# Kernel optimization log

Measured on AMD Instinct MI355X. Metric: run time of the kernel, lower is better.

## Reference

```python
import jax, jax.numpy as jnp
import numpy as np

B = 2
D = 256
NH = 8
DH = D // NH
LV = 4
NP_ = 4
NL = 6
DFF = 1024
SHAPES = [(112, 112), (56, 56), (28, 28), (14, 14)]
S = sum(h * w for h, w in SHAPES)


def setup_inputs() -> dict:
    key = jax.random.key(0)
    ks = iter(jax.random.split(key, 64))
    d = {}
    for i, (h, w) in enumerate(SHAPES):
        d[f"src{i}"] = jax.random.normal(next(ks), (B, D, h, w), jnp.float32)
        d[f"pos{i}"] = jax.random.normal(next(ks), (B, D, h, w), jnp.float32)

    def W(*shape, scale=0.02):
        return jax.random.normal(next(ks), shape, jnp.float32) * scale

    d["level_embed"] = W(LV, D, scale=1.0)
    d["off_w"] = W(NL, D, NH * LV * NP_ * 2)
    d["off_b"] = W(NL, NH * LV * NP_ * 2, scale=0.5)
    d["aw_w"] = W(NL, D, NH * LV * NP_)
    d["aw_b"] = jnp.zeros((NL, NH * LV * NP_), jnp.float32)
    d["val_w"] = W(NL, D, D)
    d["val_b"] = jnp.zeros((NL, D), jnp.float32)
    d["out_w"] = W(NL, D, D)
    d["out_b"] = jnp.zeros((NL, D), jnp.float32)
    d["ln1_s"] = jnp.ones((NL, D), jnp.float32)
    d["ln1_b"] = jnp.zeros((NL, D), jnp.float32)
    d["ff1_w"] = W(NL, D, DFF)
    d["ff1_b"] = jnp.zeros((NL, DFF), jnp.float32)
    d["ff2_w"] = W(NL, DFF, D)
    d["ff2_b"] = jnp.zeros((NL, D), jnp.float32)
    d["ln2_s"] = jnp.ones((NL, D), jnp.float32)
    d["ln2_b"] = jnp.zeros((NL, D), jnp.float32)
    return d


def _ln(x, s, b):
    m = jnp.mean(x, -1, keepdims=True)
    v = jnp.mean((x - m) ** 2, -1, keepdims=True)
    return (x - m) / jnp.sqrt(v + 1e-5) * s + b


def _bilinear(v, loc, Hl, Wl):
    # v: [N, DH, Hl, Wl]; loc: [N, Q, P, 2] in [0,1] (grid_sample align_corners=False, zero padding)
    N, Dh = v.shape[0], v.shape[1]
    Q, P = loc.shape[1], loc.shape[2]
    x = loc[..., 0] * Wl - 0.5
    y = loc[..., 1] * Hl - 0.5
    x0f = jnp.floor(x)
    y0f = jnp.floor(y)
    lx = x - x0f
    ly = y - y0f
    x0 = x0f.astype(jnp.int32)
    y0 = y0f.astype(jnp.int32)
    vf = v.reshape(N, Dh, Hl * Wl)

    def g(xi, yi):
        valid = (xi >= 0) & (xi < Wl) & (yi >= 0) & (yi < Hl)
        idx = (jnp.clip(yi, 0, Hl - 1) * Wl + jnp.clip(xi, 0, Wl - 1)).reshape(N, Q * P)
        out = jnp.take_along_axis(vf, idx[:, None, :], axis=2).reshape(N, Dh, Q, P)
        return out * valid[:, None].astype(v.dtype)

    w00 = ((1 - lx) * (1 - ly))[:, None]
    w10 = (lx * (1 - ly))[:, None]
    w01 = ((1 - lx) * ly)[:, None]
    w11 = (lx * ly)[:, None]
    return g(x0, y0) * w00 + g(x0 + 1, y0) * w10 + g(x0, y0 + 1) * w01 + g(x0 + 1, y0 + 1) * w11


def _ms_deform_attn(value, loc, attn):
    # value [B,S,NH,DH], loc [B,S,NH,LV,P,2], attn [B,S,NH,LV,P]
    out = jnp.zeros((B * NH, DH, S), value.dtype)
    s0 = 0
    for l, (Hl, Wl) in enumerate(SHAPES):
        vl = value[:, s0:s0 + Hl * Wl].reshape(B, Hl, Wl, NH, DH)
        vl = vl.transpose(0, 3, 4, 1, 2).reshape(B * NH, DH, Hl, Wl)
        ll = loc[:, :, :, l].transpose(0, 2, 1, 3, 4).reshape(B * NH, S, NP_, 2)
        al = attn[:, :, :, l].transpose(0, 2, 1, 3).reshape(B * NH, S, NP_)[:, None]
        out = out + (_bilinear(vl, ll, Hl, Wl) * al).sum(-1)
        s0 += Hl * Wl
    return out.reshape(B, NH * DH, S).transpose(0, 2, 1)


def _forward(srcs, poss, level_embed, off_w, off_b, aw_w, aw_b, val_w, val_b,
             out_w, out_b, ln1_s, ln1_b, ff1_w, ff1_b, ff2_w, ff2_b, ln2_s, ln2_b):
    src = jnp.concatenate([s.reshape(B, D, -1).transpose(0, 2, 1) for s in srcs], 1)
    pos = jnp.concatenate(
        [p.reshape(B, D, -1).transpose(0, 2, 1) + level_embed[i][None, None] for i, p in enumerate(poss)], 1)
    # reference points: padding masks are all-False => valid_ratios == 1
    refs = []
    for (Hl, Wl) in SHAPES:
        gy, gx = jnp.meshgrid((jnp.arange(Hl) + 0.5) / Hl, (jnp.arange(Wl) + 0.5) / Wl, indexing="ij")
        refs.append(jnp.stack([gx.ravel(), gy.ravel()], -1))
    ref = jnp.concatenate(refs, 0)  # [S, 2]
    normalizer = jnp.array([[w, h] for (h, w) in SHAPES], jnp.float32)  # [LV, 2] = (W, H)
    x = src
    for i in range(NL):
        q = x + pos
        off = (q @ off_w[i] + off_b[i]).reshape(B, S, NH, LV, NP_, 2)
        aw = jax.nn.softmax((q @ aw_w[i] + aw_b[i]).reshape(B, S, NH, LV * NP_), -1)
        aw = aw.reshape(B, S, NH, LV, NP_)
        val = (x @ val_w[i] + val_b[i]).reshape(B, S, NH, DH)
        loc = ref[None, :, None, None, None, :] + off / normalizer[None, None, None, :, None, :]
        attn_out = _ms_deform_attn(val, loc, aw) @ out_w[i] + out_b[i]
        x = _ln(x + attn_out, ln1_s[i], ln1_b[i])
        ff = jax.nn.relu(x @ ff1_w[i] + ff1_b[i]) @ ff2_w[i] + ff2_b[i]
        x = _ln(x + ff, ln2_s[i], ln2_b[i])
    return x


def reference(src0, src1, src2, src3, pos0, pos1, pos2, pos3, level_embed,
              off_w, off_b, aw_w, aw_b, val_w, val_b, out_w, out_b,
              ln1_s, ln1_b, ff1_w, ff1_b, ff2_w, ff2_b, ln2_s, ln2_b):
    memory = _forward([src0, src1, src2, src3], [pos0, pos1, pos2, pos3], level_embed,
                      off_w, off_b, aw_w, aw_b, val_w, val_b, out_w, out_b,
                      ln1_s, ln1_b, ff1_w, ff1_b, ff2_w, ff2_b, ln2_s, ln2_b)
    spatial_shapes = jnp.array(SHAPES, jnp.int32)
    level_start_index = jnp.concatenate(
        [jnp.zeros((1,), jnp.int32), jnp.cumsum(spatial_shapes.prod(1))[:-1].astype(jnp.int32)])
    return memory, spatial_shapes, level_start_index
```

## Files before the change

kernel.cpp:

```cpp
#include <hip/hip_runtime.h>


constexpr int kB  = 2;
constexpr int kD  = 256;
constexpr int kNH = 8;
constexpr int kLV = 4;
constexpr int kNP = 4;
constexpr int kNL = 6;
constexpr int kDFF = 1024;
constexpr int kS  = 16660;
constexpr int kM  = kB * kS;
constexpr int kMp = 33408;
constexpr int kMT64 = kMp / 64;

typedef short bf16x8 __attribute__((ext_vector_type(8)));
typedef float f32x4  __attribute__((ext_vector_type(4)));

__device__ __forceinline__ unsigned short f2bf(float x) {
  union { float f; unsigned int u; } v; v.f = x;
  unsigned int r = v.u + 0x7FFFu + ((v.u >> 16) & 1u);
  return (unsigned short)(r >> 16);
}
__device__ __forceinline__ float bf2f(unsigned short u) {
  union { unsigned int u; float f; } v; v.u = ((unsigned int)u) << 16;
  return v.f;
}
__device__ __forceinline__ float bflo(unsigned int u) {
  union { unsigned int u; float f; } v; v.u = u << 16;
  return v.f;
}
__device__ __forceinline__ float bfhi(unsigned int u) {
  union { unsigned int u; float f; } v; v.u = u & 0xFFFF0000u;
  return v.f;
}

#define GLOAD_LDS16(gp, lp)                                                    \
  __builtin_amdgcn_global_load_lds(                                            \
      (const __attribute__((address_space(1))) void*)(gp),                     \
      (__attribute__((address_space(3))) void*)(lp), 16, 0, 0)

#define SBARRIER() asm volatile("s_barrier" ::: "memory")

__global__ __launch_bounds__(256) void build_xpos_k(
    const float* __restrict__ src, const float* __restrict__ pos,
    const float* __restrict__ lemb, float* __restrict__ xout,
    unsigned short* __restrict__ posbf, unsigned short* __restrict__ xbf,
    unsigned short* __restrict__ qbf, int HW, int s0, int lvl)
{
  __shared__ float ts[32][33];
  __shared__ float tp[32][33];
  const int b  = blockIdx.z;
  const int p0 = blockIdx.x * 32, d0 = blockIdx.y * 32;
  const int tx = threadIdx.x, ty = threadIdx.y;
  for (int dd = ty; dd < 32; dd += 8) {
    int p = p0 + tx;
    if (p < HW) {
      size_t idx = ((size_t)b * kD + (d0 + dd)) * (size_t)HW + p;
      ts[dd][tx] = src[idx];
      tp[dd][tx] = pos[idx];
    }
  }
  __syncthreads();
  for (int pp = ty; pp < 32; pp += 8) {
    int p = p0 + pp, d = d0 + tx;
    if (p < HW) {
      size_t o = ((size_t)b * kS + (s0 + p)) * (size_t)kD + d;
      float x = ts[tx][pp];
      float pv = tp[tx][pp] + lemb[lvl * kD + d];
      xout[o] = x;
      posbf[o] = f2bf(pv);
      xbf[o] = f2bf(x);
      qbf[o] = f2bf(x + pv);
    }
  }
}

__global__ __launch_bounds__(256) void wconv_k(
    const float* __restrict__ W, unsigned short* __restrict__ Wt,
    int K, int N, int rowoff, int rowstotal)
{
  __shared__ float t[32][33];
  const int l = blockIdx.z;
  const int n0 = blockIdx.x * 32, k0 = blockIdx.y * 32;
  const int tx = threadIdx.x & 31, ty = threadIdx.x >> 5;
  const float* Wl = W + (size_t)l * K * N;
  unsigned short* Wtl = Wt + (size_t)l * rowstotal * K;
  for (int kk = ty; kk < 32; kk += 8)
    t[kk][tx] = Wl[(size_t)(k0 + kk) * N + n0 + tx];
  __syncthreads();
  for (int nn = ty; nn < 32; nn += 8)
    Wtl[(size_t)(rowoff + n0 + nn) * K + k0 + tx] = f2bf(t[tx][nn]);
}

__global__ __launch_bounds__(256) void biaspack_k(
    const float* __restrict__ ob, const float* __restrict__ ab,
    float* __restrict__ qb)
{
  int i = blockIdx.x * 256 + threadIdx.x;
  if (i >= kNL * 384) return;
  int l = i / 384, c = i - l * 384;
  qb[i] = (c < 256) ? ob[l * 256 + c] : ab[l * 128 + (c - 256)];
}

__global__ __launch_bounds__(256) void refxy_k(float* __restrict__ ref)
{
  int s = blockIdx.x * 256 + threadIdx.x;
  if (s >= kS) return;
  int ls, side;
  if (s < 12544)      { ls = s;         side = 112; }
  else if (s < 15680) { ls = s - 12544; side = 56;  }
  else if (s < 16464) { ls = s - 15680; side = 28;  }
  else                { ls = s - 16464; side = 14;  }
  const float inv = 1.0f / (float)side;
  ref[s * 2 + 0] = ((ls % side) + 0.5f) * inv;
  ref[s * 2 + 1] = ((ls / side) + 0.5f) * inv;
}

template<int RELU, int OUTBF>
__global__ __launch_bounds__(256) void hgemm64_k(
    const unsigned short* __restrict__ A, const unsigned short* __restrict__ Bt,
    const float* __restrict__ bias, void* __restrict__ Cout, int N, int K)
{
  __shared__ unsigned short As[2][64 * 32];
  __shared__ unsigned short Bs[2][128 * 32];
  const int tid = threadIdx.x;
  const int bm = blockIdx.y * 64;
  const int bn = blockIdx.x * 128;
  const int lane = tid & 63;
  const int wave = tid >> 6;
  const int wr = (wave >> 1) * 32, wc = (wave & 1) * 64;
  const int l15 = lane & 15, l4 = lane >> 4;

  f32x4 acc[2][4] = {};

  const unsigned short* A0 = A + (size_t)(bm + (tid >> 2)) * K + ((tid & 3) << 3);
  const int cb1 = 256 + tid;
  const unsigned short* B0 = Bt + (size_t)(bn + (tid >> 2)) * K + ((tid & 3) << 3);
  const unsigned short* B1 = Bt + (size_t)(bn + (cb1 >> 2)) * K + ((cb1 & 3) << 3);

#define STAGE64(buf, k0)                                                       \
  do {                                                                         \
    GLOAD_LDS16(A0 + (k0), (char*)As[buf] + tid * 16);                         \
    GLOAD_LDS16(B0 + (k0), (char*)Bs[buf] + tid * 16);                         \
    GLOAD_LDS16(B1 + (k0), (char*)Bs[buf] + cb1 * 16);                         \
  } while (0)

  const int nt = K >> 5;
  STAGE64(0, 0);
  STAGE64(1, 32);
  for (int k = 0; k < nt; ++k) {
    if (k + 1 < nt) asm volatile("s_waitcnt vmcnt(3)" ::: "memory");
    else            asm volatile("s_waitcnt vmcnt(0)" ::: "memory");
    SBARRIER();
    __builtin_amdgcn_sched_barrier(0);
    const int cur = k & 1;
    bf16x8 af[2], bfr[4];
#pragma unroll
    for (int m = 0; m < 2; ++m)
      af[m] = *(const bf16x8*)&As[cur][(wr + m * 16 + l15) * 32 + l4 * 8];
#pragma unroll
    for (int n = 0; n < 4; ++n)
      bfr[n] = *(const bf16x8*)&Bs[cur][(wc + n * 16 + l15) * 32 + l4 * 8];
#pragma unroll
    for (int m = 0; m < 2; ++m)
#pragma unroll
      for (int n = 0; n < 4; ++n)
        acc[m][n] = __builtin_amdgcn_mfma_f32_16x16x32_bf16(
            af[m], bfr[n], acc[m][n], 0, 0, 0);
    SBARRIER();
    if (k + 2 < nt) STAGE64(cur, (k + 2) * 32);
  }
#undef STAGE64

#pragma unroll
  for (int n = 0; n < 4; ++n) {
    const int col = bn + wc + n * 16 + l15;
    const float bv = bias[col];
#pragma unroll
    for (int m = 0; m < 2; ++m) {
#pragma unroll
      for (int j = 0; j < 4; ++j) {
        const int row = bm + wr + m * 16 + l4 * 4 + j;
        float v = acc[m][n][j] + bv;
        if (RELU) v = fmaxf(v, 0.f);
        if (OUTBF)
          ((unsigned short*)Cout)[(size_t)row * N + col] = f2bf(v);
        else
          ((float*)Cout)[(size_t)row * N + col] = v;
      }
    }
  }
}

__global__ __launch_bounds__(256) void qvgemm_k(
    const unsigned short* __restrict__ Aq, const unsigned short* __restrict__ Ax,
    const unsigned short* __restrict__ Bq, const unsigned short* __restrict__ Bv,
    const float* __restrict__ biasq, const float* __restrict__ biasv,
    _Float16* __restrict__ Cq, unsigned short* __restrict__ Cv)
{
  constexpr int K = 256;
  __shared__ unsigned short As[2][64 * 32];
  __shared__ unsigned short Bs[2][128 * 32];
  const int tid = threadIdx.x;
  const int bx = blockIdx.x;
  const bool isv = bx >= 3;
  const int bn = (isv ? bx - 3 : bx) * 128;
  const int bm = blockIdx.y * 64;
  const unsigned short* A  = isv ? Ax : Aq;
  const unsigned short* Bt = isv ? Bv : Bq;
  const float* bias = isv ? biasv : biasq;
  const int lane = tid & 63;
  const int wave = tid >> 6;
  const int wr = (wave >> 1) * 32, wc = (wave & 1) * 64;
  const int l15 = lane & 15, l4 = lane >> 4;

  f32x4 acc[2][4] = {};

  const unsigned short* A0 = A + (size_t)(bm + (tid >> 2)) * K + ((tid & 3) << 3);
  const int cb1 = 256 + tid;
  const unsigned short* B0 = Bt + (size_t)(bn + (tid >> 2)) * K + ((tid & 3) << 3);
  const unsigned short* B1 = Bt + (size_t)(bn + (cb1 >> 2)) * K + ((cb1 & 3) << 3);

#define STAGEQV(buf, k0)                                                       \
  do {                                                                         \
    GLOAD_LDS16(A0 + (k0), (char*)As[buf] + tid * 16);                         \
    GLOAD_LDS16(B0 + (k0), (char*)Bs[buf] + tid * 16);                         \
    GLOAD_LDS16(B1 + (k0), (char*)Bs[buf] + cb1 * 16);                         \
  } while (0)

  const int nt = K >> 5;
  STAGEQV(0, 0);
  STAGEQV(1, 32);
  for (int k = 0; k < nt; ++k) {
    if (k + 1 < nt) asm volatile("s_waitcnt vmcnt(3)" ::: "memory");
    else            asm volatile("s_waitcnt vmcnt(0)" ::: "memory");
    SBARRIER();
    __builtin_amdgcn_sched_barrier(0);
    const int cur = k & 1;
    bf16x8 af[2], bfr[4];
#pragma unroll
    for (int m = 0; m < 2; ++m)
      af[m] = *(const bf16x8*)&As[cur][(wr + m * 16 + l15) * 32 + l4 * 8];
#pragma unroll
    for (int n = 0; n < 4; ++n)
      bfr[n] = *(const bf16x8*)&Bs[cur][(wc + n * 16 + l15) * 32 + l4 * 8];
#pragma unroll
    for (int m = 0; m < 2; ++m)
#pragma unroll
      for (int n = 0; n < 4; ++n)
        acc[m][n] = __builtin_amdgcn_mfma_f32_16x16x32_bf16(
            af[m], bfr[n], acc[m][n], 0, 0, 0);
    SBARRIER();
    if (k + 2 < nt) STAGEQV(cur, (k + 2) * 32);
  }
#undef STAGEQV

#pragma unroll
  for (int n = 0; n < 4; ++n) {
    const int col = bn + wc + n * 16 + l15;
    const float bv = bias[col];
#pragma unroll
    for (int m = 0; m < 2; ++m) {
#pragma unroll
      for (int j = 0; j < 4; ++j) {
        const int row = bm + wr + m * 16 + l4 * 4 + j;
        float v = acc[m][n][j] + bv;
        if (isv)
          Cv[(size_t)row * 256 + col] = f2bf(v);
        else
          Cq[(size_t)row * 384 + col] = (_Float16)v;
      }
    }
  }
}

template<int WQ, int OUTDST>
__global__ __launch_bounds__(512) void hgemmln_k(
    const unsigned short* __restrict__ A, const unsigned short* __restrict__ Bt,
    const float* __restrict__ bias, const float* __restrict__ Rsd,
    const float* __restrict__ g, const float* __restrict__ beta,
    const unsigned short* __restrict__ posbf, float* __restrict__ yout,
    unsigned short* __restrict__ xbf, unsigned short* __restrict__ qbf, int K)
{
  __shared__ unsigned short As[2][64 * 32];
  __shared__ unsigned short Bs[2][256 * 32];
  float* ssum = (float*)&As[0][0];
  float* ssq  = ssum + 64 * 5;
  const int tid = threadIdx.x;
  const int bm = blockIdx.x * 64;
  const int lane = tid & 63;
  const int wave = tid >> 6;
  const int wm = wave >> 2;
  const int wn = wave & 3;
  const int wc = wn * 64;
  const int l15 = lane & 15, l4 = lane >> 4;

  f32x4 acc[2][4] = {};

  const unsigned short* Aq = A + (size_t)(bm + (tid >> 2)) * K + ((tid & 3) << 3);
  const unsigned short* Bq0 = Bt + (size_t)(tid >> 2) * K + ((tid & 3) << 3);
  const unsigned short* Bq1 = Bt + (size_t)(128 + (tid >> 2)) * K + ((tid & 3) << 3);

#define STAGE_LN(buf, k0)                                                      \
  do {                                                                         \
    if (tid < 256) GLOAD_LDS16(Aq + (k0), (char*)As[buf] + tid * 16);          \
    GLOAD_LDS16(Bq0 + (k0), (char*)Bs[buf] + tid * 16);                        \
    GLOAD_LDS16(Bq1 + (k0), (char*)Bs[buf] + (512 + tid) * 16);                \
  } while (0)

  const int nt = K >> 5;
  STAGE_LN(0, 0);
  STAGE_LN(1, 32);
  for (int k = 0; k < nt; ++k) {
    if (k + 1 < nt) {
      if (wave < 4) asm volatile("s_waitcnt vmcnt(3)" ::: "memory");
      else          asm volatile("s_waitcnt vmcnt(2)" ::: "memory");
    } else {
      asm volatile("s_waitcnt vmcnt(0)" ::: "memory");
    }
    SBARRIER();
    __builtin_amdgcn_sched_barrier(0);
    const int cur = k & 1;
    bf16x8 af[2], bfr[4];
#pragma unroll
    for (int m = 0; m < 2; ++m)
      af[m] = *(const bf16x8*)&As[cur][(wm * 32 + m * 16 + l15) * 32 + l4 * 8];
#pragma unroll
    for (int n = 0; n < 4; ++n)
      bfr[n] = *(const bf16x8*)&Bs[cur][(wc + n * 16 + l15) * 32 + l4 * 8];
#pragma unroll
    for (int m = 0; m < 2; ++m)
#pragma unroll
      for (int n = 0; n < 4; ++n)
        acc[m][n] = __builtin_amdgcn_mfma_f32_16x16x32_bf16(
            af[m], bfr[n], acc[m][n], 0, 0, 0);
    SBARRIER();
    if (k + 2 < nt) STAGE_LN(cur, (k + 2) * 32);
  }
#undef STAGE_LN

  float bv[4], gv[4], btv[4];
#pragma unroll
  for (int n = 0; n < 4; ++n) {
    const int col = wc + n * 16 + l15;
    bv[n] = bias[col];
    gv[n] = g[col];
    btv[n] = beta[col];
  }
#pragma unroll
  for (int m = 0; m < 2; ++m) {
#pragma unroll
    for (int j = 0; j < 4; ++j) {
      const int row = bm + wm * 32 + m * 16 + l4 * 4 + j;
#pragma unroll
      for (int n = 0; n < 4; ++n)
        acc[m][n][j] += bv[n] + Rsd[(size_t)row * kD + wc + n * 16 + l15];
    }
  }
#pragma unroll
  for (int m = 0; m < 2; ++m) {
#pragma unroll
    for (int j = 0; j < 4; ++j) {
      float s = acc[m][0][j] + acc[m][1][j] + acc[m][2][j] + acc[m][3][j];
      float q = acc[m][0][j] * acc[m][0][j] + acc[m][1][j] * acc[m][1][j] +
                acc[m][2][j] * acc[m][2][j] + acc[m][3][j] * acc[m][3][j];
#pragma unroll
      for (int d2 = 1; d2 < 16; d2 <<= 1) {
        s += __shfl_xor(s, d2, 64);
        q += __shfl_xor(q, d2, 64);
      }
      if (l15 == 0) {
        const int r = wm * 32 + m * 16 + l4 * 4 + j;
        ssum[r * 5 + wn] = s;
        ssq[r * 5 + wn] = q;
      }
    }
  }
  __syncthreads();
#pragma unroll
  for (int m = 0; m < 2; ++m) {
#pragma unroll
    for (int j = 0; j < 4; ++j) {
      const int r = wm * 32 + m * 16 + l4 * 4 + j;
      const int row = bm + r;
      const float mean = (ssum[r * 5 + 0] + ssum[r * 5 + 1] + ssum[r * 5 + 2] +
                          ssum[r * 5 + 3]) * (1.0f / kD);
      const float var = (ssq[r * 5 + 0] + ssq[r * 5 + 1] + ssq[r * 5 + 2] +
                         ssq[r * 5 + 3]) * (1.0f / kD) - mean * mean;
      const float rstd = rsqrtf(var + 1e-5f);
      if (row < kM) {
#pragma unroll
        for (int n = 0; n < 4; ++n) {
          const int col = wc + n * 16 + l15;
          const float y = (acc[m][n][j] - mean) * rstd * gv[n] + btv[n];
          const size_t o = (size_t)row * kD + col;
          if (OUTDST) {
            yout[o] = y;
          } else {
            yout[o] = y;
            xbf[o] = f2bf(y);
            if (WQ) qbf[o] = f2bf(y + bf2f(posbf[o]));
          }
        }
      }
    }
  }
}

__global__ __launch_bounds__(256) void msdeform_k(
    const unsigned short* __restrict__ val, const _Float16* __restrict__ qout,
    const float* __restrict__ ref, unsigned short* __restrict__ outbf)
{
  __shared__ int   sIdx[4][8][128];
  __shared__ float sW[4][8][128];
  const int bid = blockIdx.x;
  const int xcd = bid & 7;
  const int jj  = bid >> 3;
  const int wg  = (xcd < 5 ? xcd * 521 : 5 * 521 + (xcd - 5) * 520) + jj;
  const int bs0 = wg * 8;
  const int tid = threadIdx.x;

#pragma unroll
  for (int it = 0; it < 4; ++it) {
    const int item = tid + it * 256;
    const int q = item >> 7;
    const int t = item & 127;
    const int bs = bs0 + q;
    const int b = bs / kS, s = bs - b * kS;
    const int l = (t & 15) >> 2;

    const float logit = (float)qout[(size_t)bs * 384 + 256 + t];
    float mx = logit;
#pragma unroll
    for (int d2 = 1; d2 < 16; d2 <<= 1) mx = fmaxf(mx, __shfl_xor(mx, d2, 64));
    float e = __expf(logit - mx);
    float sm = e;
#pragma unroll
    for (int d2 = 1; d2 < 16; d2 <<= 1) sm += __shfl_xor(sm, d2, 64);
    const float a = e / sm;

    const float rfx = ref[s * 2 + 0];
    const float rfy = ref[s * 2 + 1];
    const int side  = 112 >> l;
    const int start = (l >= 1 ? 12544 : 0) + (l >= 2 ? 3136 : 0) + (l >= 3 ? 784 : 0);
    const float ox = (float)qout[(size_t)bs * 384 + t * 2 + 0];
    const float oy = (float)qout[(size_t)bs * 384 + t * 2 + 1];
    const float xx = fmaf(rfx, (float)side, ox) - 0.5f;
    const float yy = fmaf(rfy, (float)side, oy) - 0.5f;
    const float xf = floorf(xx), yf = floorf(yy);
    const float lx = xx - xf, ly = yy - yf;
    const int x0 = (int)xf, y0 = (int)yf;
    const float w00 = (1.f - lx) * (1.f - ly) * a, w10 = lx * (1.f - ly) * a;
    const float w01 = (1.f - lx) * ly * a,         w11 = lx * ly * a;
    const bool xv0 = (unsigned)x0 < (unsigned)side, xv1 = (unsigned)(x0 + 1) < (unsigned)side;
    const bool yv0 = (unsigned)y0 < (unsigned)side, yv1 = (unsigned)(y0 + 1) < (unsigned)side;
    const int cx0 = min(max(x0, 0), side - 1), cx1 = min(max(x0 + 1, 0), side - 1);
    const int cy0 = min(max(y0, 0), side - 1), cy1 = min(max(y0 + 1, 0), side - 1);
    const int rowbase = b * kS + start;
    const int t2 = (t & 15) * 8 + (t >> 4);
    sIdx[0][q][t2] = (rowbase + cy0 * side + cx0) << 9;
    sIdx[1][q][t2] = (rowbase + cy0 * side + cx1) << 9;
    sIdx[2][q][t2] = (rowbase + cy1 * side + cx0) << 9;
    sIdx[3][q][t2] = (rowbase + cy1 * side + cx1) << 9;
    sW[0][q][t2] = (xv0 && yv0) ? w00 : 0.f;
    sW[1][q][t2] = (xv1 && yv0) ? w10 : 0.f;
    sW[2][q][t2] = (xv0 && yv1) ? w01 : 0.f;
    sW[3][q][t2] = (xv1 && yv1) ? w11 : 0.f;
  }
  __syncthreads();

  const int q  = tid >> 5;
  const int h  = (tid >> 2) & 7;
  const int l4 = tid & 3;
  const char* vbase = (const char*)val + h * 64 + l4 * 16;

  float a0 = 0.f, a1 = 0.f, a2 = 0.f, a3 = 0.f;
  float a4 = 0.f, a5 = 0.f, a6 = 0.f, a7 = 0.f;
#pragma unroll
  for (int sp = 0; sp < 16; ++sp) {
    const int t2 = sp * 8 + h;
#pragma unroll
    for (int c = 0; c < 4; ++c) {
      const int off = sIdx[c][q][t2];
      const float w = sW[c][q][t2];
      const uint4 v = *(const uint4*)(vbase + off);
      a0 = fmaf(w, bflo(v.x), a0); a1 = fmaf(w, bfhi(v.x), a1);
      a2 = fmaf(w, bflo(v.y), a2); a3 = fmaf(w, bfhi(v.y), a3);
      a4 = fmaf(w, bflo(v.z), a4); a5 = fmaf(w, bfhi(v.z), a5);
      a6 = fmaf(w, bflo(v.w), a6); a7 = fmaf(w, bfhi(v.w), a7);
    }
  }
  bf16x8 o;
  o[0] = (short)f2bf(a0); o[1] = (short)f2bf(a1);
  o[2] = (short)f2bf(a2); o[3] = (short)f2bf(a3);
  o[4] = (short)f2bf(a4); o[5] = (short)f2bf(a5);
  o[6] = (short)f2bf(a6); o[7] = (short)f2bf(a7);
  *(bf16x8*)(outbf + (size_t)(bs0 + q) * 256 + h * 32 + l4 * 8) = o;
}

__global__ void tail_k(float* __restrict__ out)
{
  if (threadIdx.x == 0) {
    const size_t n = (size_t)kM * kD;
    out[n + 0] = 112.f; out[n + 1] = 112.f;
    out[n + 2] = 56.f;  out[n + 3] = 56.f;
    out[n + 4] = 28.f;  out[n + 5] = 28.f;
    out[n + 6] = 14.f;  out[n + 7] = 14.f;
    out[n + 8] = 0.f;   out[n + 9] = 12544.f;
    out[n + 10] = 15680.f; out[n + 11] = 16464.f;
  }
}

extern "C" void kernel_launch(void* const* d_in, const int* in_sizes, int n_in,
                              void* d_out, int out_size, void* d_ws, size_t ws_size,
                              hipStream_t stream)
{
  const float* src[4] = {(const float*)d_in[0], (const float*)d_in[2],
                         (const float*)d_in[4], (const float*)d_in[6]};
  const float* pos[4] = {(const float*)d_in[1], (const float*)d_in[3],
                         (const float*)d_in[5], (const float*)d_in[7]};
  const float* lemb  = (const float*)d_in[8];
  const float* off_w = (const float*)d_in[9];
  const float* off_b = (const float*)d_in[10];
  const float* aw_w  = (const float*)d_in[11];
  const float* aw_b  = (const float*)d_in[12];
  const float* val_w = (const float*)d_in[13];
  const float* val_b = (const float*)d_in[14];
  const float* out_w = (const float*)d_in[15];
  const float* out_b = (const float*)d_in[16];
  const float* ln1_s = (const float*)d_in[17];
  const float* ln1_b = (const float*)d_in[18];
  const float* ff1_w = (const float*)d_in[19];
  const float* ff1_b = (const float*)d_in[20];
  const float* ff2_w = (const float*)d_in[21];
  const float* ff2_b = (const float*)d_in[22];
  const float* ln2_s = (const float*)d_in[23];
  const float* ln2_b = (const float*)d_in[24];

  const size_t SZ = (size_t)kMp * kD;
  float* ws   = (float*)d_ws;
  float* xb   = ws;
  _Float16* qoutH = (_Float16*)(ws + SZ);
  unsigned short* valbf = (unsigned short*)(ws + SZ + (3 * SZ) / 4);
  unsigned short* attbf = valbf + SZ;
  unsigned short* ffbf  = (unsigned short*)(ws + SZ);
  unsigned short* posbf = (unsigned short*)(ws + 3 * SZ);
  unsigned short* qbf   = posbf + SZ;
  unsigned short* xbf   = qbf + SZ;
  unsigned short* wts   = (unsigned short*)(ws + 4 * SZ + SZ / 2);
  unsigned short* qwT  = wts;
  unsigned short* valT = qwT + kNL * 384 * 256;
  unsigned short* outT = valT + kNL * 256 * 256;
  unsigned short* ff1T = outT + kNL * 256 * 256;
  unsigned short* ff2T = ff1T + kNL * 1024 * 256;
  float* qbias = (float*)(ff2T + kNL * 256 * 1024);
  float* reftab = qbias + kNL * 384;

  wconv_k<<<dim3(256 / 32, 256 / 32, kNL), 256, 0, stream>>>(off_w, qwT, 256, 256, 0, 384);
  wconv_k<<<dim3(128 / 32, 256 / 32, kNL), 256, 0, stream>>>(aw_w,  qwT, 256, 128, 256, 384);
  wconv_k<<<dim3(256 / 32, 256 / 32, kNL), 256, 0, stream>>>(val_w, valT, 256, 256, 0, 256);
  wconv_k<<<dim3(256 / 32, 256 / 32, kNL), 256, 0, stream>>>(out_w, outT, 256, 256, 0, 256);
  wconv_k<<<dim3(1024 / 32, 256 / 32, kNL), 256, 0, stream>>>(ff1_w, ff1T, 256, 1024, 0, 1024);
  wconv_k<<<dim3(256 / 32, 1024 / 32, kNL), 256, 0, stream>>>(ff2_w, ff2T, 1024, 256, 0, 256);
  biaspack_k<<<(kNL * 384 + 255) / 256, 256, 0, stream>>>(off_b, aw_b, qbias);
  refxy_k<<<(kS + 255) / 256, 256, 0, stream>>>(reftab);

  const int sides[4]  = {112, 56, 28, 14};
  const int starts[4] = {0, 12544, 15680, 16464};
  for (int l = 0; l < 4; ++l) {
    int HW = sides[l] * sides[l];
    dim3 g((HW + 31) / 32, kD / 32, kB);
    build_xpos_k<<<g, dim3(32, 8), 0, stream>>>(src[l], pos[l], lemb, xb, posbf,
                                                xbf, qbf, HW, starts[l], l);
  }

  const dim3 blk(256);
  for (int i = 0; i < kNL; ++i) {
    qvgemm_k<<<dim3(5, kMT64), blk, 0, stream>>>(
        qbf, xbf, qwT + (size_t)i * 384 * 256, valT + (size_t)i * 256 * 256,
        qbias + i * 384, val_b + i * 256, qoutH, valbf);
    msdeform_k<<<kM / 8, blk, 0, stream>>>(valbf, qoutH, reftab, attbf);
    hgemmln_k<0, 0><<<kMT64, 512, 0, stream>>>(
        attbf, outT + (size_t)i * 256 * 256, out_b + i * 256, xb,
        ln1_s + i * kD, ln1_b + i * kD, nullptr, xb, xbf, nullptr, 256);
    hgemm64_k<1, 1><<<dim3(8, kMT64), blk, 0, stream>>>(
        xbf, ff1T + (size_t)i * 1024 * 256, ff1_b + i * 1024, ffbf, 1024, 256);
    if (i < kNL - 1) {
      hgemmln_k<1, 0><<<kMT64, 512, 0, stream>>>(
          ffbf, ff2T + (size_t)i * 256 * 1024, ff2_b + i * 256, xb,
          ln2_s + i * kD, ln2_b + i * kD, posbf, xb, xbf, qbf, 1024);
    } else {
      hgemmln_k<0, 1><<<kMT64, 512, 0, stream>>>(
          ffbf, ff2T + (size_t)i * 256 * 1024, ff2_b + i * 256, xb,
          ln2_s + i * kD, ln2_b + i * kD, nullptr, (float*)d_out, nullptr,
          nullptr, 1024);
    }
  }

  tail_k<<<1, 64, 0, stream>>>((float*)d_out);
}
```

Baseline: 1.357 ms.

## Deepen hgemmln K-loop pipeline to four LDS stages with split MFMA phases

The GEMM+LayerNorm kernel moves from a double-buffered to a four-stage LDS ring, issuing global-to-LDS loads up to three k-steps ahead with computed vmcnt waits. Each k-step is split into two MFMA phases separated by barriers, with explicit lgkmcnt waits and setprio raised around the MFMA bursts so waves interleave memory and compute. This aims to hide global load latency better. In exchange it doubles the shared memory footprint, which may lower occupancy, and adds more barriers per iteration.

Measured after the change: 1.410 ms. 3.9% more time.

```diff
diff --git a/kernel.cpp b/kernel.cpp
--- a/kernel.cpp
+++ b/kernel.cpp
@@ -40,6 +40,22 @@
       (__attribute__((address_space(3))) void*)(lp), 16, 0, 0)
 
 #define SBARRIER() asm volatile("s_barrier" ::: "memory")
+#define LGKM0()                                                                \
+  do {                                                                         \
+    asm volatile("s_waitcnt lgkmcnt(0)" ::: "memory");                         \
+    __builtin_amdgcn_sched_barrier(0);                                         \
+  } while (0)
+
+__device__ __forceinline__ void vmwait(int n) {
+  switch (n) {
+    case 0: asm volatile("s_waitcnt vmcnt(0)" ::: "memory"); break;
+    case 2: asm volatile("s_waitcnt vmcnt(2)" ::: "memory"); break;
+    case 3: asm volatile("s_waitcnt vmcnt(3)" ::: "memory"); break;
+    case 4: asm volatile("s_waitcnt vmcnt(4)" ::: "memory"); break;
+    case 6: asm volatile("s_waitcnt vmcnt(6)" ::: "memory"); break;
+    default: asm volatile("s_waitcnt vmcnt(9)" ::: "memory"); break;
+  }
+}
 
 __global__ __launch_bounds__(256) void build_xpos_k(
     const float* __restrict__ src, const float* __restrict__ pos,
@@ -282,8 +298,8 @@
     const unsigned short* __restrict__ posbf, float* __restrict__ yout,
     unsigned short* __restrict__ xbf, unsigned short* __restrict__ qbf, int K)
 {
-  __shared__ unsigned short As[2][64 * 32];
-  __shared__ unsigned short Bs[2][256 * 32];
+  __shared__ unsigned short As[4][64 * 32];
+  __shared__ unsigned short Bs[4][256 * 32];
   float* ssum = (float*)&As[0][0];
   float* ssq  = ssum + 64 * 5;
   const int tid = threadIdx.x;
@@ -301,43 +317,87 @@
   const unsigned short* Bq0 = Bt + (size_t)(tid >> 2) * K + ((tid & 3) << 3);
   const unsigned short* Bq1 = Bt + (size_t)(128 + (tid >> 2)) * K + ((tid & 3) << 3);
 
-#define STAGE_LN(buf, k0)                                                      \
+#define ISSUE(h)                                                               \
   do {                                                                         \
-    if (tid < 256) GLOAD_LDS16(Aq + (k0), (char*)As[buf] + tid * 16);          \
-    GLOAD_LDS16(Bq0 + (k0), (char*)Bs[buf] + tid * 16);                        \
-    GLOAD_LDS16(Bq1 + (k0), (char*)Bs[buf] + (512 + tid) * 16);                \
+    const int _s = (h) & 3;                                                    \
+    const int _k = (h) * 32;                                                   \
+    GLOAD_LDS16(Bq0 + _k, (char*)Bs[_s] + tid * 16);                           \
+    GLOAD_LDS16(Bq1 + _k, (char*)Bs[_s] + (512 + tid) * 16);                   \
+    if (tid < 256) GLOAD_LDS16(Aq + _k, (char*)As[_s] + tid * 16);             \
   } while (0)
 
-  const int nt = K >> 5;
-  STAGE_LN(0, 0);
-  STAGE_LN(1, 32);
-  for (int k = 0; k < nt; ++k) {
-    if (k + 1 < nt) {
-      if (wave < 4) asm volatile("s_waitcnt vmcnt(3)" ::: "memory");
-      else          asm volatile("s_waitcnt vmcnt(2)" ::: "memory");
-    } else {
-      asm volatile("s_waitcnt vmcnt(0)" ::: "memory");
-    }
-    SBARRIER();
+  const int NT = K >> 6;
+  const int HL = 2 * NT - 1;
+  const int Lw = (wave < 4) ? 3 : 2;
+
+  ISSUE(0);
+  ISSUE(1);
+  ISSUE(2);
+
+  for (int T = 0; T < NT; ++T) {
+    const int h0 = 2 * T, h1 = 2 * T + 1;
+    const int s0 = h0 & 3, s1 = h1 & 3;
+    bf16x8 af0, af1, b0, b1, b2, b3;
+
+    if (h0 + 3 <= HL) ISSUE(h0 + 3);
+    vmwait(((h0 + 3 <= HL ? h0 + 3 : HL) - h0) * Lw);
+    SBARRIER();
+    af0 = *(const bf16x8*)&As[s0][(wm * 32 + 0 * 16 + l15) * 32 + l4 * 8];
+    af1 = *(const bf16x8*)&As[s0][(wm * 32 + 1 * 16 + l15) * 32 + l4 * 8];
+    b0  = *(const bf16x8*)&Bs[s0][(wc + 0 * 16 + l15) * 32 + l4 * 8];
+    b1  = *(const bf16x8*)&Bs[s0][(wc + 1 * 16 + l15) * 32 + l4 * 8];
+    LGKM0();
+    __builtin_amdgcn_s_setprio(1);
+    acc[0][0] = __builtin_amdgcn_mfma_f32_16x16x32_bf16(af0, b0, acc[0][0], 0, 0, 0);
+    acc[1][0] = __builtin_amdgcn_mfma_f32_16x16x32_bf16(af1, b0, acc[1][0], 0, 0, 0);
+    acc[0][1] = __builtin_amdgcn_mfma_f32_16x16x32_bf16(af0, b1, acc[0][1], 0, 0, 0);
+    acc[1][1] = __builtin_amdgcn_mfma_f32_16x16x32_bf16(af1, b1, acc[1][1], 0, 0, 0);
+    __builtin_amdgcn_s_setprio(0);
     __builtin_amdgcn_sched_barrier(0);
-    const int cur = k & 1;
-    bf16x8 af[2], bfr[4];
-#pragma unroll
-    for (int m = 0; m < 2; ++m)
-      af[m] = *(const bf16x8*)&As[cur][(wm * 32 + m * 16 + l15) * 32 + l4 * 8];
-#pragma unroll
-    for (int n = 0; n < 4; ++n)
-      bfr[n] = *(const bf16x8*)&Bs[cur][(wc + n * 16 + l15) * 32 + l4 * 8];
-#pragma unroll
-    for (int m = 0; m < 2; ++m)
-#pragma unroll
-      for (int n = 0; n < 4; ++n)
-        acc[m][n] = __builtin_amdgcn_mfma_f32_16x16x32_bf16(
-            af[m], bfr[n], acc[m][n], 0, 0, 0);
-    SBARRIER();
-    if (k + 2 < nt) STAGE_LN(cur, (k + 2) * 32);
-  }
-#undef STAGE_LN
+    SBARRIER();
+
+    b2 = *(const bf16x8*)&Bs[s0][(wc + 2 * 16 + l15) * 32 + l4 * 8];
+    b3 = *(const bf16x8*)&Bs[s0][(wc + 3 * 16 + l15) * 32 + l4 * 8];
+    LGKM0();
+    __builtin_amdgcn_s_setprio(1);
+    acc[0][2] = __builtin_amdgcn_mfma_f32_16x16x32_bf16(af0, b2, acc[0][2], 0, 0, 0);
+    acc[1][2] = __builtin_amdgcn_mfma_f32_16x16x32_bf16(af1, b2, acc[1][2], 0, 0, 0);
+    acc[0][3] = __builtin_amdgcn_mfma_f32_16x16x32_bf16(af0, b3, acc[0][3], 0, 0, 0);
+    acc[1][3] = __builtin_amdgcn_mfma_f32_16x16x32_bf16(af1, b3, acc[1][3], 0, 0, 0);
+    __builtin_amdgcn_s_setprio(0);
+    __builtin_amdgcn_sched_barrier(0);
+    SBARRIER();
+
+    if (h0 + 4 <= HL) ISSUE(h0 + 4);
+    vmwait(((h0 + 4 <= HL ? h0 + 4 : HL) - h1) * Lw);
+    SBARRIER();
+    af0 = *(const bf16x8*)&As[s1][(wm * 32 + 0 * 16 + l15) * 32 + l4 * 8];
+    af1 = *(const bf16x8*)&As[s1][(wm * 32 + 1 * 16 + l15) * 32 + l4 * 8];
+    b0  = *(const bf16x8*)&Bs[s1][(wc + 0 * 16 + l15) * 32 + l4 * 8];
+    b1  = *(const bf16x8*)&Bs[s1][(wc + 1 * 16 + l15) * 32 + l4 * 8];
+    LGKM0();
+    __builtin_amdgcn_s_setprio(1);
+    acc[0][0] = __builtin_amdgcn_mfma_f32_16x16x32_bf16(af0, b0, acc[0][0], 0, 0, 0);
+    acc[1][0] = __builtin_amdgcn_mfma_f32_16x16x32_bf16(af1, b0, acc[1][0], 0, 0, 0);
+    acc[0][1] = __builtin_amdgcn_mfma_f32_16x16x32_bf16(af0, b1, acc[0][1], 0, 0, 0);
+    acc[1][1] = __builtin_amdgcn_mfma_f32_16x16x32_bf16(af1, b1, acc[1][1], 0, 0, 0);
+    __builtin_amdgcn_s_setprio(0);
+    __builtin_amdgcn_sched_barrier(0);
+    SBARRIER();
+
+    b2 = *(const bf16x8*)&Bs[s1][(wc + 2 * 16 + l15) * 32 + l4 * 8];
+    b3 = *(const bf16x8*)&Bs[s1][(wc + 3 * 16 + l15) * 32 + l4 * 8];
+    LGKM0();
+    __builtin_amdgcn_s_setprio(1);
+    acc[0][2] = __builtin_amdgcn_mfma_f32_16x16x32_bf16(af0, b2, acc[0][2], 0, 0, 0);
+    acc[1][2] = __builtin_amdgcn_mfma_f32_16x16x32_bf16(af1, b2, acc[1][2], 0, 0, 0);
+    acc[0][3] = __builtin_amdgcn_mfma_f32_16x16x32_bf16(af0, b3, acc[0][3], 0, 0, 0);
+    acc[1][3] = __builtin_amdgcn_mfma_f32_16x16x32_bf16(af1, b3, acc[1][3], 0, 0, 0);
+    __builtin_amdgcn_s_setprio(0);
+    __builtin_amdgcn_sched_barrier(0);
+    SBARRIER();
+  }
+#undef ISSUE
 
   float bv[4], gv[4], btv[4];
 #pragma unroll
```

## Load GEMM-LN A fragments directly to registers and unroll K loop by two

Applied to the files above, without the earlier changes.

In the GEMM+LayerNorm kernel, the A operand is no longer staged through LDS. Each wave now loads its bf16x8 A fragments straight from global memory into registers, double-buffered across even and odd K steps, while B keeps its async global-to-LDS staging. The K loop is manually unrolled by two with fixed buffers and uniform vmcnt waits. This removes LDS traffic and the per-wave split waits for A, at the cost of uncoalesced A loads and more live registers.

Measured after the change: 1.486 ms. +9.6%, slower.

```diff
diff --git a/kernel.cpp b/kernel.cpp
--- a/kernel.cpp
+++ b/kernel.cpp
@@ -282,10 +282,9 @@
     const unsigned short* __restrict__ posbf, float* __restrict__ yout,
     unsigned short* __restrict__ xbf, unsigned short* __restrict__ qbf, int K)
 {
-  __shared__ unsigned short As[2][64 * 32];
   __shared__ unsigned short Bs[2][256 * 32];
-  float* ssum = (float*)&As[0][0];
-  float* ssq  = ssum + 64 * 5;
+  __shared__ float ssum[64][5];
+  __shared__ float ssq[64][5];
   const int tid = threadIdx.x;
   const int bm = blockIdx.x * 64;
   const int lane = tid & 63;
@@ -297,47 +296,69 @@
 
   f32x4 acc[2][4] = {};
 
-  const unsigned short* Aq = A + (size_t)(bm + (tid >> 2)) * K + ((tid & 3) << 3);
   const unsigned short* Bq0 = Bt + (size_t)(tid >> 2) * K + ((tid & 3) << 3);
   const unsigned short* Bq1 = Bt + (size_t)(128 + (tid >> 2)) * K + ((tid & 3) << 3);
-
-#define STAGE_LN(buf, k0)                                                      \
+  const unsigned short* A0p = A + (size_t)(bm + wm * 32 + l15) * K + l4 * 8;
+  const unsigned short* A1p = A0p + (size_t)16 * K;
+
+#define STB(buf, k0)                                                           \
   do {                                                                         \
-    if (tid < 256) GLOAD_LDS16(Aq + (k0), (char*)As[buf] + tid * 16);          \
     GLOAD_LDS16(Bq0 + (k0), (char*)Bs[buf] + tid * 16);                        \
     GLOAD_LDS16(Bq1 + (k0), (char*)Bs[buf] + (512 + tid) * 16);                \
   } while (0)
 
+#define COMPUTE(buf, aa0, aa1)                                                 \
+  do {                                                                         \
+    bf16x8 b0 = *(const bf16x8*)&Bs[buf][(wc + 0 * 16 + l15) * 32 + l4 * 8];   \
+    bf16x8 b1 = *(const bf16x8*)&Bs[buf][(wc + 1 * 16 + l15) * 32 + l4 * 8];   \
+    bf16x8 b2 = *(const bf16x8*)&Bs[buf][(wc + 2 * 16 + l15) * 32 + l4 * 8];   \
+    bf16x8 b3 = *(const bf16x8*)&Bs[buf][(wc + 3 * 16 + l15) * 32 + l4 * 8];   \
+    acc[0][0] = __builtin_amdgcn_mfma_f32_16x16x32_bf16(aa0, b0, acc[0][0], 0, 0, 0); \
+    acc[1][0] = __builtin_amdgcn_mfma_f32_16x16x32_bf16(aa1, b0, acc[1][0], 0, 0, 0); \
+    acc[0][1] = __builtin_amdgcn_mfma_f32_16x16x32_bf16(aa0, b1, acc[0][1], 0, 0, 0); \
+    acc[1][1] = __builtin_amdgcn_mfma_f32_16x16x32_bf16(aa1, b1, acc[1][1], 0, 0, 0); \
+    acc[0][2] = __builtin_amdgcn_mfma_f32_16x16x32_bf16(aa0, b2, acc[0][2], 0, 0, 0); \
+    acc[1][2] = __builtin_amdgcn_mfma_f32_16x16x32_bf16(aa1, b2, acc[1][2], 0, 0, 0); \
+    acc[0][3] = __builtin_amdgcn_mfma_f32_16x16x32_bf16(aa0, b3, acc[0][3], 0, 0, 0); \
+    acc[1][3] = __builtin_amdgcn_mfma_f32_16x16x32_bf16(aa1, b3, acc[1][3], 0, 0, 0); \
+  } while (0)
+
   const int nt = K >> 5;
-  STAGE_LN(0, 0);
-  STAGE_LN(1, 32);
-  for (int k = 0; k < nt; ++k) {
-    if (k + 1 < nt) {
-      if (wave < 4) asm volatile("s_waitcnt vmcnt(3)" ::: "memory");
-      else          asm volatile("s_waitcnt vmcnt(2)" ::: "memory");
-    } else {
-      asm volatile("s_waitcnt vmcnt(0)" ::: "memory");
-    }
+  bf16x8 aE0, aE1, aO0, aO1;
+
+  STB(0, 0);
+  aE0 = *(const bf16x8*)(A0p + 0);
+  aE1 = *(const bf16x8*)(A1p + 0);
+  STB(1, 32);
+  aO0 = *(const bf16x8*)(A0p + 32);
+  aO1 = *(const bf16x8*)(A1p + 32);
+
+  for (int k = 0; k < nt; k += 2) {
+    if (k + 1 < nt) asm volatile("s_waitcnt vmcnt(4)" ::: "memory");
+    else            asm volatile("s_waitcnt vmcnt(0)" ::: "memory");
     SBARRIER();
     __builtin_amdgcn_sched_barrier(0);
-    const int cur = k & 1;
-    bf16x8 af[2], bfr[4];
-#pragma unroll
-    for (int m = 0; m < 2; ++m)
-      af[m] = *(const bf16x8*)&As[cur][(wm * 32 + m * 16 + l15) * 32 + l4 * 8];
-#pragma unroll
-    for (int n = 0; n < 4; ++n)
-      bfr[n] = *(const bf16x8*)&Bs[cur][(wc + n * 16 + l15) * 32 + l4 * 8];
-#pragma unroll
-    for (int m = 0; m < 2; ++m)
-#pragma unroll
-      for (int n = 0; n < 4; ++n)
-        acc[m][n] = __builtin_amdgcn_mfma_f32_16x16x32_bf16(
-            af[m], bfr[n], acc[m][n], 0, 0, 0);
-    SBARRIER();
-    if (k + 2 < nt) STAGE_LN(cur, (k + 2) * 32);
-  }
-#undef STAGE_LN
+    COMPUTE(0, aE0, aE1);
+    SBARRIER();
+    if (k + 2 < nt) {
+      STB(0, (k + 2) * 32);
+      aE0 = *(const bf16x8*)(A0p + (k + 2) * 32);
+      aE1 = *(const bf16x8*)(A1p + (k + 2) * 32);
+    }
+    if (k + 2 < nt) asm volatile("s_waitcnt vmcnt(4)" ::: "memory");
+    else            asm volatile("s_waitcnt vmcnt(0)" ::: "memory");
+    SBARRIER();
+    __builtin_amdgcn_sched_barrier(0);
+    COMPUTE(1, aO0, aO1);
+    SBARRIER();
+    if (k + 3 < nt) {
+      STB(1, (k + 3) * 32);
+      aO0 = *(const bf16x8*)(A0p + (k + 3) * 32);
+      aO1 = *(const bf16x8*)(A1p + (k + 3) * 32);
+    }
+  }
+#undef STB
+#undef COMPUTE
 
   float bv[4], gv[4], btv[4];
 #pragma unroll
@@ -371,8 +392,8 @@
       }
       if (l15 == 0) {
         const int r = wm * 32 + m * 16 + l4 * 4 + j;
-        ssum[r * 5 + wn] = s;
-        ssq[r * 5 + wn] = q;
+        ssum[r][wn] = s;
+        ssq[r][wn] = q;
       }
     }
   }
@@ -383,10 +404,10 @@
     for (int j = 0; j < 4; ++j) {
       const int r = wm * 32 + m * 16 + l4 * 4 + j;
       const int row = bm + r;
-      const float mean = (ssum[r * 5 + 0] + ssum[r * 5 + 1] + ssum[r * 5 + 2] +
-                          ssum[r * 5 + 3]) * (1.0f / kD);
-      const float var = (ssq[r * 5 + 0] + ssq[r * 5 + 1] + ssq[r * 5 + 2] +
-                         ssq[r * 5 + 3]) * (1.0f / kD) - mean * mean;
+      const float mean = (ssum[r][0] + ssum[r][1] + ssum[r][2] + ssum[r][3]) *
+                         (1.0f / kD);
+      const float var = (ssq[r][0] + ssq[r][1] + ssq[r][2] + ssq[r][3]) *
+                        (1.0f / kD) - mean * mean;
       const float rstd = rsqrtf(var + 1e-5f);
       if (row < kM) {
 #pragma unroll
```
